# Kernel tuning notes

Measured on AMD Instinct MI355X. Metric: run time of the kernel, lower is better.

The kernel has to match this reference:

```python
import jax, jax.numpy as jnp
from jax import lax
import numpy as np

EPS = 1e-5
K = 3


def _conv(x, w, b, pad, dil=1, groups=1):
    out = lax.conv_general_dilated(
        x, w, (1, 1), [(pad, pad), (pad, pad)], rhs_dilation=(dil, dil),
        dimension_numbers=('NCHW', 'OIHW', 'NCHW'), feature_group_count=groups)
    return out + b[None, :, None, None]


def _bn(x, g, b, m, v):
    scale = g / jnp.sqrt(v + EPS)
    return (x - m[None, :, None, None]) * scale[None, :, None, None] + b[None, :, None, None]


def setup_inputs() -> dict:
    key = jax.random.key(0)
    ks = jax.random.split(key, 24)
    B, C, H, W = 8, 256, 48, 80
    Hd = 256  # hidden_channels
    n = lambda k, s, sc=0.05: (jax.random.normal(k, s, dtype=jnp.float32) * sc)
    return {
        'f_t_minus_2': jax.random.normal(ks[0], (B, C, H, W), dtype=jnp.float32),
        'f_t_minus_1': jax.random.normal(ks[1], (B, C, H, W), dtype=jnp.float32),
        'f_t':         jax.random.normal(ks[2], (B, C, H, W), dtype=jnp.float32),
        'ov_w1': n(ks[3], (Hd, 3 * C, 3, 3)), 'ov_b1': n(ks[4], (Hd,)),
        'bn1_g': jnp.ones((Hd,), jnp.float32), 'bn1_b': jnp.zeros((Hd,), jnp.float32),
        'bn1_m': n(ks[5], (Hd,)), 'bn1_v': jax.random.uniform(ks[6], (Hd,), jnp.float32, 0.5, 1.5),
        'ov_w2': n(ks[7], (Hd, Hd, 3, 3)), 'ov_b2': n(ks[8], (Hd,)),
        'bn2_g': jnp.ones((Hd,), jnp.float32), 'bn2_b': jnp.zeros((Hd,), jnp.float32),
        'bn2_m': n(ks[9], (Hd,)), 'bn2_v': jax.random.uniform(ks[10], (Hd,), jnp.float32, 0.5, 1.5),
        'g_w': n(ks[11], (C, Hd, 1, 1)), 'g_b': n(ks[12], (C,)),
        'fc1_w': n(ks[13], (512, 2 * C)), 'fc1_b': n(ks[14], (512,)),
        'fc2_w': n(ks[15], (C * K * K, 512)), 'fc2_b': n(ks[16], (C * K * K,)),
        'ap_w': n(ks[17], (1, 2 * C, 1, 1)), 'ap_b': n(ks[18], (1,)),
        'a_w': n(ks[19], (1, 2 * C, 1, 1)), 'a_b': jnp.ones((1,), jnp.float32),
    }


def reference(f_t_minus_2, f_t_minus_1, f_t,
              ov_w1, ov_b1, bn1_g, bn1_b, bn1_m, bn1_v,
              ov_w2, ov_b2, bn2_g, bn2_b, bn2_m, bn2_v,
              g_w, g_b, fc1_w, fc1_b, fc2_w, fc2_b,
              ap_w, ap_b, a_w, a_b):
    B, C, H, W = f_t.shape
    # (1) Overview-Net (GCM)
    f_concat = jnp.concatenate([f_t_minus_2, f_t_minus_1, f_t], axis=1)
    h = jax.nn.relu(_bn(_conv(f_concat, ov_w1, ov_b1, pad=2, dil=2), bn1_g, bn1_b, bn1_m, bn1_v))
    h = jax.nn.relu(_bn(_conv(h, ov_w2, ov_b2, pad=4, dil=4), bn2_g, bn2_b, bn2_m, bn2_v))
    g_pooled = h.mean(axis=(2, 3), keepdims=True)            # [B,Hd,1,1]
    G = _conv(g_pooled, g_w, g_b, pad=0)                     # [B,C,1,1]
    # (2) Focus-Net: FC-generated per-(batch,channel) 3x3 depthwise conv on (f_t, f_{t-1})
    Fs = jnp.concatenate([f_t, f_t_minus_1], axis=0)         # [2B,C,H,W]
    g_flat = jnp.repeat(G.reshape(B, C), 2, axis=0)          # [2B,C]
    gap = Fs.mean(axis=(2, 3))                               # [2B,C]
    fc_in = jnp.concatenate([g_flat, gap], axis=1)           # [2B,2C]
    w = jax.nn.silu(fc_in @ fc1_w.T + fc1_b) @ fc2_w.T + fc2_b  # [2B, C*9]
    w = w.reshape(2 * B * C, 1, K, K)
    x = Fs.reshape(1, 2 * B * C, H, W)
    out = lax.conv_general_dilated(
        x, w, (1, 1), [(1, 1), (1, 1)],
        dimension_numbers=('NCHW', 'OIHW', 'NCHW'), feature_group_count=2 * B * C)
    out = out.reshape(2 * B, C, H, W)
    f_t_mod, f_t1_mod = out[:B], out[B:]
    # (3) Dynamic fusion
    f_prev_cat = jnp.concatenate([f_t1_mod, f_t_minus_2], axis=1)
    alpha_prev = 0.3 + 0.4 * jax.nn.sigmoid(_conv(f_prev_cat, ap_w, ap_b, pad=0))
    f_prev = alpha_prev * f_t1_mod + (1.0 - alpha_prev) * f_t_minus_2
    f_cat = jnp.concatenate([f_t_mod, f_prev], axis=1)
    alpha = 0.6 + 0.3 * jax.nn.sigmoid(_conv(f_cat, a_w, a_b, pad=0))
    return alpha * f_t_mod + (1.0 - alpha) * f_prev
```

## Files before the change

kernel.cpp:

```cpp
#include <hip/hip_runtime.h>
#include <hip/hip_bf16.h>
#include <math.h>


typedef __bf16 bf16x8 __attribute__((ext_vector_type(8)));
typedef float f32x4 __attribute__((ext_vector_type(4)));
typedef __attribute__((address_space(1))) void as1_void;
typedef __attribute__((address_space(3))) void as3_void;


__global__ __launch_bounds__(256) void prep_consts_kernel(
    const float* __restrict__ ob1, const float* __restrict__ g1, const float* __restrict__ b1,
    const float* __restrict__ m1, const float* __restrict__ v1,
    const float* __restrict__ ob2, const float* __restrict__ g2, const float* __restrict__ b2,
    const float* __restrict__ m2, const float* __restrict__ v2,
    float* __restrict__ cst)
{
  int i = threadIdx.x;
  float a1 = g1[i] / sqrtf(v1[i] + 1e-5f);
  cst[i]       = a1;
  cst[256 + i] = (ob1[i] - m1[i]) * a1 + b1[i];
  float a2 = g2[i] / sqrtf(v2[i] + 1e-5f);
  cst[512 + i] = a2;
  cst[768 + i] = (ob2[i] - m2[i]) * a2 + b2[i];
}

__global__ __launch_bounds__(256) void pad_concat_kernel(
    const float* __restrict__ f2, const float* __restrict__ f1, const float* __restrict__ f0,
    __hip_bfloat16* __restrict__ out)
{
  int bid = blockIdx.x;
  const int cg = bid % 6; bid /= 6;
  const int y = bid % 48;
  const int b = bid / 48;

  __shared__ float tile[128 * 85];

  const float* src = (cg < 2) ? f2 : ((cg < 4) ? f1 : f0);
  const int ccbase = (cg & 1) * 128;

#pragma unroll
  for (int it = 0; it < 10; it++) {
    const int idx = it * 256 + threadIdx.x;
    const int cl = idx / 20, x4 = idx % 20;
    const float4 v = *(const float4*)(src +
        (((size_t)b * 256 + ccbase + cl) * 48 + y) * 80 + x4 * 4);
    float* t = tile + cl * 85 + x4 * 4;
    t[0] = v.x; t[1] = v.y; t[2] = v.z; t[3] = v.w;
  }
  __syncthreads();

  __hip_bfloat16* obase = out + ((size_t)(b * 52 + y + 2) * 84 + 2) * 768 + cg * 128;
#pragma unroll
  for (int it = 0; it < 5; it++) {
    const int idx = it * 256 + threadIdx.x;
    const int chunk = idx & 15, x = idx >> 4;
    const float* t = tile + chunk * 8 * 85 + x;
    union { __hip_bfloat16 h[8]; uint4 u; } pk;
#pragma unroll
    for (int j = 0; j < 8; j++) pk.h[j] = __float2bfloat16(t[j * 85]);
    *(uint4*)(obase + (size_t)x * 768 + chunk * 8) = pk.u;
  }
}

__global__ __launch_bounds__(256) void repack_w_kernel(
    const float* __restrict__ w, __hip_bfloat16* __restrict__ out, int OC, int IC)
{
  int idx = blockIdx.x * 256 + threadIdx.x;
  if (idx >= OC * IC * 9) return;
  int ic = idx % IC;
  int t = idx / IC;
  int oc = t % OC;
  int tap = t / OC;
  out[idx] = __float2bfloat16(w[(oc * IC + ic) * 9 + tap]);
}

__global__ __launch_bounds__(256) void gap_kernel(
    const float* __restrict__ f0, const float* __restrict__ f1, float* __restrict__ gapv)
{
  int i = blockIdx.x >> 8, c = blockIdx.x & 255;
  const float* src = (i < 8) ? (f0 + ((size_t)i * 256 + c) * 3840)
                             : (f1 + ((size_t)(i - 8) * 256 + c) * 3840);
  float s = 0.f;
  for (int k = threadIdx.x; k < 3840; k += 256) s += src[k];
  for (int off = 32; off; off >>= 1) s += __shfl_xor(s, off);
  __shared__ float red[4];
  if ((threadIdx.x & 63) == 0) red[threadIdx.x >> 6] = s;
  __syncthreads();
  if (threadIdx.x == 0)
    gapv[blockIdx.x] = (red[0] + red[1] + red[2] + red[3]) * (1.f / 3840.f);
}

template <int CIN, int HP, int WP, int DIL, int MODE>
__global__ __launch_bounds__(256) void conv_mfma_kernel(
    const __hip_bfloat16* __restrict__ inp, const __hip_bfloat16* __restrict__ wt,
    const float* __restrict__ bnA, const float* __restrict__ bnB,
    __hip_bfloat16* __restrict__ outp, float* __restrict__ gpool)
{
  __shared__ unsigned short As[8192] __attribute__((aligned(16)));
  __shared__ unsigned short Bs[8192] __attribute__((aligned(16)));

  int bid = blockIdx.x;
  bid = (bid & 7) * 60 + (bid >> 3);
  const int ocb = bid & 1; bid >>= 1;
  const int xb = bid % 5; bid /= 5;
  const int yb = bid % 6; bid /= 6;
  const int b = bid;
  const int y0 = yb * 8, x0 = xb * 16, oc0 = ocb * 128;

  const int t = threadIdx.x;
  const int w = t >> 6, l = t & 63;
  const int col16 = l & 15, quad = l >> 4;
  const int wm = w >> 1, wn = w & 1;
  const int rsub = l >> 3;
  const int jj = (l & 7) ^ rsub;

  f32x4 acc[4][4];
  const f32x4 zf = {0.f, 0.f, 0.f, 0.f};
#pragma unroll
  for (int i = 0; i < 4; i++)
#pragma unroll
    for (int j = 0; j < 4; j++) acc[i][j] = zf;

  for (int c0 = 0; c0 < CIN; c0 += 64) {
    for (int tap = 0; tap < 9; tap++) {
      const int ty = tap / 3, tx = tap - ty * 3;
      const __hip_bfloat16* inBase =
          inp + ((size_t)(b * HP + y0 + DIL * ty) * WP + (x0 + DIL * tx)) * CIN + jj * 8 + c0;
      const __hip_bfloat16* wBase = wt + (size_t)(tap * 256 + oc0) * CIN + jj * 8 + c0;
      __syncthreads();
#pragma unroll
      for (int i = 0; i < 4; i++) {
        const int q = i * 4 + w;
        const int m = q * 8 + rsub;
        const int ry = m >> 4, rx = m & 15;
        const __hip_bfloat16* gp = inBase + (ry * WP + rx) * CIN;
        __builtin_amdgcn_global_load_lds((as1_void*)gp,
            (as3_void*)((char*)As + q * 1024), 16, 0, 0);
      }
#pragma unroll
      for (int i = 0; i < 4; i++) {
        const int q = i * 4 + w;
        const int n = q * 8 + rsub;
        const __hip_bfloat16* gp = wBase + n * CIN;
        __builtin_amdgcn_global_load_lds((as1_void*)gp,
            (as3_void*)((char*)Bs + q * 1024), 16, 0, 0);
      }
      __syncthreads();
#pragma unroll
      for (int kiter = 0; kiter < 2; kiter++) {
        bf16x8 af[4], bg[4];
#pragma unroll
        for (int fi = 0; fi < 4; fi++) {
          const int m = wm * 64 + fi * 16 + col16;
          const int jc = (kiter * 4 + quad) ^ (m & 7);
          af[fi] = *(const bf16x8*)((const char*)As + m * 128 + jc * 16);
        }
#pragma unroll
        for (int fi = 0; fi < 4; fi++) {
          const int n = wn * 64 + fi * 16 + col16;
          const int jc = (kiter * 4 + quad) ^ (n & 7);
          bg[fi] = *(const bf16x8*)((const char*)Bs + n * 128 + jc * 16);
        }
#pragma unroll
        for (int fm_ = 0; fm_ < 4; fm_++)
#pragma unroll
          for (int fn_ = 0; fn_ < 4; fn_++)
            acc[fm_][fn_] = __builtin_amdgcn_mfma_f32_16x16x32_bf16(
                af[fm_], bg[fn_], acc[fm_][fn_], 0, 0, 0);
      }
    }
  }

  if (MODE == 0) {
#pragma unroll
    for (int fn_ = 0; fn_ < 4; fn_++) {
      const int oc = oc0 + wn * 64 + fn_ * 16 + col16;
      const float sa = bnA[oc], sb = bnB[oc];
#pragma unroll
      for (int fm_ = 0; fm_ < 4; fm_++) {
#pragma unroll
        for (int r = 0; r < 4; r++) {
          const int m = wm * 64 + fm_ * 16 + quad * 4 + r;
          const int y = y0 + (m >> 4), x = x0 + (m & 15);
          const float v = fmaxf(acc[fm_][fn_][r] * sa + sb, 0.f);
          outp[((size_t)(b * 56 + y + 4) * 88 + (x + 4)) * 256 + oc] = __float2bfloat16(v);
        }
      }
    }
  } else {
#pragma unroll
    for (int fn_ = 0; fn_ < 4; fn_++) {
      const int oc = oc0 + wn * 64 + fn_ * 16 + col16;
      const float sa = bnA[oc], sb = bnB[oc];
      float cs = 0.f;
#pragma unroll
      for (int fm_ = 0; fm_ < 4; fm_++)
#pragma unroll
        for (int r = 0; r < 4; r++)
          cs += fmaxf(acc[fm_][fn_][r] * sa + sb, 0.f);
      cs += __shfl_xor(cs, 16);
      cs += __shfl_xor(cs, 32);
      if (quad == 0) atomicAdd(&gpool[b * 256 + oc], cs);
    }
  }
}


__global__ __launch_bounds__(256) void fcG_kernel(
    const float* __restrict__ gpool, const float* __restrict__ gw,
    const float* __restrict__ gb, float* __restrict__ G)
{
  int b = blockIdx.x, oc = threadIdx.x;
  __shared__ float pool[256];
  pool[oc] = gpool[b * 256 + oc] * (1.f / 3840.f);
  __syncthreads();
  float s = gb[oc];
  const float* wr = gw + oc * 256;
  for (int c2 = 0; c2 < 256; c2++) s += pool[c2] * wr[c2];
  G[b * 256 + oc] = s;
}

__global__ __launch_bounds__(256) void fc1_kernel(
    const float* __restrict__ G, const float* __restrict__ gapv,
    const float* __restrict__ w, const float* __restrict__ bias,
    float* __restrict__ out1)
{
  __shared__ float fin[16][513];
  for (int idx = threadIdx.x; idx < 16 * 512; idx += 256) {
    int i = idx >> 9, k = idx & 511;
    fin[i][k] = (k < 256) ? G[(i >> 1) * 256 + k] : gapv[i * 256 + (k - 256)];
  }
  __syncthreads();
  int g = blockIdx.x * 256 + threadIdx.x;
  int j = g >> 4, i = g & 15;
  float s = bias[j];
  const float* wr = w + j * 512;
  for (int k = 0; k < 512; k++) s += fin[i][k] * wr[k];
  out1[j * 16 + i] = s / (1.f + expf(-s));
}

__global__ __launch_bounds__(256) void fc2_kernel(
    const float* __restrict__ out1, const float* __restrict__ w,
    const float* __restrict__ bias, float* __restrict__ wdw)
{
  __shared__ float fin[16][513];
  for (int idx = threadIdx.x; idx < 16 * 512; idx += 256) {
    int i = idx >> 9, k = idx & 511;
    fin[i][k] = out1[k * 16 + i];
  }
  __syncthreads();
  int g = blockIdx.x * 256 + threadIdx.x;
  int j = g >> 4, i = g & 15;
  float s = bias[j];
  const float* wr = w + j * 512;
  for (int k = 0; k < 512; k++) s += fin[i][k] * wr[k];
  wdw[i * 2304 + j] = s;
}

__global__ __launch_bounds__(256) void dw_kernel(
    const float* __restrict__ f0, const float* __restrict__ f1,
    const float* __restrict__ wdw, float* __restrict__ fm)
{
  int i = blockIdx.x >> 8, c = blockIdx.x & 255;
  const float* src = (i < 8) ? (f0 + ((size_t)i * 256 + c) * 3840)
                             : (f1 + ((size_t)(i - 8) * 256 + c) * 3840);
  float* dst = fm + ((size_t)i * 256 + c) * 3840;
  __shared__ float w9[9];
  if (threadIdx.x < 9) w9[threadIdx.x] = wdw[i * 2304 + c * 9 + threadIdx.x];
  __syncthreads();
  for (int p = threadIdx.x; p < 3840; p += 256) {
    int y = p / 80, x = p - y * 80;
    float s = 0.f;
#pragma unroll
    for (int ky = 0; ky < 3; ky++) {
      int yy = y + ky - 1;
      if (yy < 0 || yy >= 48) continue;
#pragma unroll
      for (int kx = 0; kx < 3; kx++) {
        int xx = x + kx - 1;
        if (xx < 0 || xx >= 80) continue;
        s += w9[ky * 3 + kx] * src[yy * 80 + xx];
      }
    }
    dst[p] = s;
  }
}

__global__ __launch_bounds__(320) void alpha_final_kernel(
    const float* __restrict__ fm, const float* __restrict__ f2,
    const float* __restrict__ apw, const float* __restrict__ apb,
    const float* __restrict__ aw, const float* __restrict__ ab,
    float* __restrict__ out)
{
  int b = blockIdx.x / 48, y = blockIdx.x % 48;
  int x = threadIdx.x % 80, g = threadIdx.x / 80;
  const float* ftm  = fm + ((size_t)b * 256) * 3840 + y * 80 + x;
  const float* ft1m = fm + ((size_t)(b + 8) * 256) * 3840 + y * 80 + x;
  const float* ptm2 = f2 + ((size_t)b * 256) * 3840 + y * 80 + x;
  float S = 0.f, T0 = 0.f, T1 = 0.f, T2 = 0.f;
  for (int cc = 0; cc < 64; cc++) {
    int c = g * 64 + cc;
    float v1 = ft1m[(size_t)c * 3840];
    float v2 = ptm2[(size_t)c * 3840];
    float v0 = ftm[(size_t)c * 3840];
    S  += apw[c] * v1 + apw[256 + c] * v2;
    T0 += aw[c] * v0;
    T1 += aw[256 + c] * v1;
    T2 += aw[256 + c] * v2;
  }
  __shared__ float red[4][4][80];
  __shared__ float apl[80], all[80];
  red[0][g][x] = S; red[1][g][x] = T0; red[2][g][x] = T1; red[3][g][x] = T2;
  __syncthreads();
  if (g == 0) {
    S  = red[0][0][x] + red[0][1][x] + red[0][2][x] + red[0][3][x];
    T0 = red[1][0][x] + red[1][1][x] + red[1][2][x] + red[1][3][x];
    T1 = red[2][0][x] + red[2][1][x] + red[2][2][x] + red[2][3][x];
    T2 = red[3][0][x] + red[3][1][x] + red[3][2][x] + red[3][3][x];
    float ap = 0.3f + 0.4f / (1.f + expf(-(S + apb[0])));
    float A  = T0 + ap * T1 + (1.f - ap) * T2 + ab[0];
    float al = 0.6f + 0.3f / (1.f + expf(-A));
    apl[x] = ap; all[x] = al;
  }
  __syncthreads();
  const float ap = apl[x], al = all[x];
  float* ob = out + ((size_t)b * 256) * 3840 + y * 80 + x;
  for (int cc = 0; cc < 64; cc++) {
    size_t off = (size_t)(g * 64 + cc) * 3840;
    float v0 = ftm[off], v1 = ft1m[off], v2 = ptm2[off];
    ob[off] = al * v0 + (1.f - al) * (ap * v1 + (1.f - ap) * v2);
  }
}


extern "C" void kernel_launch(void* const* d_in, const int* in_sizes, int n_in,
                              void* d_out, int out_size, void* d_ws, size_t ws_size,
                              hipStream_t stream)
{
  const float* f_tm2 = (const float*)d_in[0];
  const float* f_tm1 = (const float*)d_in[1];
  const float* f_t   = (const float*)d_in[2];
  const float* ov_w1 = (const float*)d_in[3];
  const float* ov_b1 = (const float*)d_in[4];
  const float* bn1_g = (const float*)d_in[5];
  const float* bn1_b = (const float*)d_in[6];
  const float* bn1_m = (const float*)d_in[7];
  const float* bn1_v = (const float*)d_in[8];
  const float* ov_w2 = (const float*)d_in[9];
  const float* ov_b2 = (const float*)d_in[10];
  const float* bn2_g = (const float*)d_in[11];
  const float* bn2_b = (const float*)d_in[12];
  const float* bn2_m = (const float*)d_in[13];
  const float* bn2_v = (const float*)d_in[14];
  const float* g_w   = (const float*)d_in[15];
  const float* g_b   = (const float*)d_in[16];
  const float* fc1_w = (const float*)d_in[17];
  const float* fc1_b = (const float*)d_in[18];
  const float* fc2_w = (const float*)d_in[19];
  const float* fc2_b = (const float*)d_in[20];
  const float* ap_w  = (const float*)d_in[21];
  const float* ap_b  = (const float*)d_in[22];
  const float* a_w   = (const float*)d_in[23];
  const float* a_b   = (const float*)d_in[24];

  char* ws = (char*)d_ws;
  float* fm            = (float*)ws;
  __hip_bfloat16* in1p = (__hip_bfloat16*)ws;
  __hip_bfloat16* wt1  = (__hip_bfloat16*)(ws + 53673984);
  __hip_bfloat16* wt2  = (__hip_bfloat16*)(ws + 57212928);
  __hip_bfloat16* h1p  = (__hip_bfloat16*)(ws + 58392576);
  float* gpool         = (float*)(ws + 78577664);
  float* gapv          = (float*)(ws + 78585856);
  float* Gv            = (float*)(ws + 78602240);
  float* out1          = (float*)(ws + 78610432);
  float* wdw           = (float*)(ws + 78643200);
  float* cst           = (float*)(ws + 79036416);

  hipMemsetAsync(in1p, 0, 53673984, stream);
  hipMemsetAsync(h1p, 0, 20185088, stream);
  hipMemsetAsync(gpool, 0, 8192, stream);

  prep_consts_kernel<<<1, 256, 0, stream>>>(ov_b1, bn1_g, bn1_b, bn1_m, bn1_v,
                                            ov_b2, bn2_g, bn2_b, bn2_m, bn2_v, cst);
  pad_concat_kernel<<<2304, 256, 0, stream>>>(f_tm2, f_tm1, f_t, in1p);
  repack_w_kernel<<<6912, 256, 0, stream>>>(ov_w1, wt1, 256, 768);
  repack_w_kernel<<<2304, 256, 0, stream>>>(ov_w2, wt2, 256, 256);
  gap_kernel<<<4096, 256, 0, stream>>>(f_t, f_tm1, gapv);

  conv_mfma_kernel<768, 52, 84, 2, 0><<<480, 256, 0, stream>>>(in1p, wt1, cst, cst + 256, h1p, nullptr);
  conv_mfma_kernel<256, 56, 88, 4, 1><<<480, 256, 0, stream>>>(h1p, wt2, cst + 512, cst + 768, nullptr, gpool);

  fcG_kernel<<<8, 256, 0, stream>>>(gpool, g_w, g_b, Gv);
  fc1_kernel<<<32, 256, 0, stream>>>(Gv, gapv, fc1_w, fc1_b, out1);
  fc2_kernel<<<144, 256, 0, stream>>>(out1, fc2_w, fc2_b, wdw);
  dw_kernel<<<4096, 256, 0, stream>>>(f_t, f_tm1, wdw, fm);
  alpha_final_kernel<<<384, 320, 0, stream>>>(fm, f_tm2, ap_w, ap_b, a_w, a_b, (float*)d_out);
}
```

Before: 528.9 us.

## Fuse GAP into pad_concat, zero only borders, cache alpha inputs in registers

Drops the full 53MB memset of the padded input buffer. pad_concat now zeroes only the border columns and rows it owns, and also computes the spatial sums of f_t and f_{t-1} per channel with atomics. This removes the separate gap_kernel pass over those tensors. The final alpha kernel now uses 640 threads and keeps its 32-channel slice in registers, so the three inputs are not read twice from global memory. The risks are higher register pressure, and the gpool memset now covers gapv, which depends on the workspace layout staying contiguous.

```diff
diff --git a/kernel.cpp b/kernel.cpp
--- a/kernel.cpp
+++ b/kernel.cpp
@@ -27,7 +27,7 @@
 
 __global__ __launch_bounds__(256) void pad_concat_kernel(
     const float* __restrict__ f2, const float* __restrict__ f1, const float* __restrict__ f0,
-    __hip_bfloat16* __restrict__ out)
+    __hip_bfloat16* __restrict__ out, float* __restrict__ gapv)
 {
   int bid = blockIdx.x;
   const int cg = bid % 6; bid /= 6;
@@ -38,6 +38,7 @@
 
   const float* src = (cg < 2) ? f2 : ((cg < 4) ? f1 : f0);
   const int ccbase = (cg & 1) * 128;
+  const uint4 z4 = {0u, 0u, 0u, 0u};
 
 #pragma unroll
   for (int it = 0; it < 10; it++) {
@@ -48,6 +49,20 @@
     float* t = tile + cl * 85 + x4 * 4;
     t[0] = v.x; t[1] = v.y; t[2] = v.z; t[3] = v.w;
   }
+
+  if (threadIdx.x < 32) {
+    const int xb_ = threadIdx.x >> 3, ch8 = threadIdx.x & 7;
+    const int xx = (xb_ < 2) ? xb_ : (80 + xb_);
+    *(uint4*)(out + ((size_t)(b * 52 + y + 2) * 84 + xx) * 768 + cg * 128 + ch8 * 8) = z4;
+  }
+  if (y == 0 || y == 47) {
+    const int r0 = (y == 0) ? 0 : 50;
+    for (int idx = threadIdx.x; idx < 1344; idx += 256) {
+      const int rr = idx / 672, rem = idx % 672;
+      const int xx = rem >> 3, ch8 = rem & 7;
+      *(uint4*)(out + ((size_t)(b * 52 + r0 + rr) * 84 + xx) * 768 + cg * 128 + ch8 * 8) = z4;
+    }
+  }
   __syncthreads();
 
   __hip_bfloat16* obase = out + ((size_t)(b * 52 + y + 2) * 84 + 2) * 768 + cg * 128;
@@ -60,6 +75,17 @@
 #pragma unroll
     for (int j = 0; j < 8; j++) pk.h[j] = __float2bfloat16(t[j * 85]);
     *(uint4*)(obase + (size_t)x * 768 + chunk * 8) = pk.u;
+  }
+
+  if (cg >= 2) {
+    const int i_gap = (cg >= 4) ? b : (b + 8);
+    const int cl = threadIdx.x >> 1, half = threadIdx.x & 1;
+    const float* t = tile + cl * 85 + half * 40;
+    float s = 0.f;
+#pragma unroll
+    for (int k = 0; k < 40; k++) s += t[k];
+    s += __shfl_xor(s, 1);
+    if (half == 0) atomicAdd(&gapv[i_gap * 256 + ccbase + cl], s);
   }
 }
 
@@ -73,22 +99,6 @@
   int oc = t % OC;
   int tap = t / OC;
   out[idx] = __float2bfloat16(w[(oc * IC + ic) * 9 + tap]);
-}
-
-__global__ __launch_bounds__(256) void gap_kernel(
-    const float* __restrict__ f0, const float* __restrict__ f1, float* __restrict__ gapv)
-{
-  int i = blockIdx.x >> 8, c = blockIdx.x & 255;
-  const float* src = (i < 8) ? (f0 + ((size_t)i * 256 + c) * 3840)
-                             : (f1 + ((size_t)(i - 8) * 256 + c) * 3840);
-  float s = 0.f;
-  for (int k = threadIdx.x; k < 3840; k += 256) s += src[k];
-  for (int off = 32; off; off >>= 1) s += __shfl_xor(s, off);
-  __shared__ float red[4];
-  if ((threadIdx.x & 63) == 0) red[threadIdx.x >> 6] = s;
-  __syncthreads();
-  if (threadIdx.x == 0)
-    gapv[blockIdx.x] = (red[0] + red[1] + red[2] + red[3]) * (1.f / 3840.f);
 }
 
 template <int CIN, int HP, int WP, int DIL, int MODE>
@@ -229,7 +239,8 @@
   __shared__ float fin[16][513];
   for (int idx = threadIdx.x; idx < 16 * 512; idx += 256) {
     int i = idx >> 9, k = idx & 511;
-    fin[i][k] = (k < 256) ? G[(i >> 1) * 256 + k] : gapv[i * 256 + (k - 256)];
+    fin[i][k] = (k < 256) ? G[(i >> 1) * 256 + k]
+                          : gapv[i * 256 + (k - 256)] * (1.f / 3840.f);
   }
   __syncthreads();
   int g = blockIdx.x * 256 + threadIdx.x;
@@ -287,7 +298,7 @@
   }
 }
 
-__global__ __launch_bounds__(320) void alpha_final_kernel(
+__global__ __launch_bounds__(640) void alpha_final_kernel(
     const float* __restrict__ fm, const float* __restrict__ f2,
     const float* __restrict__ apw, const float* __restrict__ apb,
     const float* __restrict__ aw, const float* __restrict__ ab,
@@ -295,42 +306,44 @@
 {
   int b = blockIdx.x / 48, y = blockIdx.x % 48;
   int x = threadIdx.x % 80, g = threadIdx.x / 80;
-  const float* ftm  = fm + ((size_t)b * 256) * 3840 + y * 80 + x;
-  const float* ft1m = fm + ((size_t)(b + 8) * 256) * 3840 + y * 80 + x;
-  const float* ptm2 = f2 + ((size_t)b * 256) * 3840 + y * 80 + x;
+  const float* ftm  = fm + ((size_t)(b * 256) + g * 32) * 3840 + y * 80 + x;
+  const float* ft1m = fm + ((size_t)((b + 8) * 256) + g * 32) * 3840 + y * 80 + x;
+  const float* ptm2 = f2 + ((size_t)(b * 256) + g * 32) * 3840 + y * 80 + x;
+
+  float v0[32], v1[32], v2[32];
   float S = 0.f, T0 = 0.f, T1 = 0.f, T2 = 0.f;
-  for (int cc = 0; cc < 64; cc++) {
-    int c = g * 64 + cc;
-    float v1 = ft1m[(size_t)c * 3840];
-    float v2 = ptm2[(size_t)c * 3840];
-    float v0 = ftm[(size_t)c * 3840];
-    S  += apw[c] * v1 + apw[256 + c] * v2;
-    T0 += aw[c] * v0;
-    T1 += aw[256 + c] * v1;
-    T2 += aw[256 + c] * v2;
-  }
-  __shared__ float red[4][4][80];
-  __shared__ float apl[80], all[80];
+#pragma unroll
+  for (int cc = 0; cc < 32; cc++) {
+    v0[cc] = ftm[(size_t)cc * 3840];
+    v1[cc] = ft1m[(size_t)cc * 3840];
+    v2[cc] = ptm2[(size_t)cc * 3840];
+    const int c = g * 32 + cc;
+    S  += apw[c] * v1[cc] + apw[256 + c] * v2[cc];
+    T0 += aw[c] * v0[cc];
+    T1 += aw[256 + c] * v1[cc];
+    T2 += aw[256 + c] * v2[cc];
+  }
+  __shared__ float red[4][8][80];
+  __shared__ float apl[80], alb[80];
   red[0][g][x] = S; red[1][g][x] = T0; red[2][g][x] = T1; red[3][g][x] = T2;
   __syncthreads();
   if (g == 0) {
-    S  = red[0][0][x] + red[0][1][x] + red[0][2][x] + red[0][3][x];
-    T0 = red[1][0][x] + red[1][1][x] + red[1][2][x] + red[1][3][x];
-    T1 = red[2][0][x] + red[2][1][x] + red[2][2][x] + red[2][3][x];
-    T2 = red[3][0][x] + red[3][1][x] + red[3][2][x] + red[3][3][x];
-    float ap = 0.3f + 0.4f / (1.f + expf(-(S + apb[0])));
-    float A  = T0 + ap * T1 + (1.f - ap) * T2 + ab[0];
+    float s = 0.f, t0 = 0.f, t1 = 0.f, t2 = 0.f;
+#pragma unroll
+    for (int k = 0; k < 8; k++) {
+      s += red[0][k][x]; t0 += red[1][k][x]; t1 += red[2][k][x]; t2 += red[3][k][x];
+    }
+    float ap = 0.3f + 0.4f / (1.f + expf(-(s + apb[0])));
+    float A  = t0 + ap * t1 + (1.f - ap) * t2 + ab[0];
     float al = 0.6f + 0.3f / (1.f + expf(-A));
-    apl[x] = ap; all[x] = al;
-  }
-  __syncthreads();
-  const float ap = apl[x], al = all[x];
-  float* ob = out + ((size_t)b * 256) * 3840 + y * 80 + x;
-  for (int cc = 0; cc < 64; cc++) {
-    size_t off = (size_t)(g * 64 + cc) * 3840;
-    float v0 = ftm[off], v1 = ft1m[off], v2 = ptm2[off];
-    ob[off] = al * v0 + (1.f - al) * (ap * v1 + (1.f - ap) * v2);
-  }
+    apl[x] = ap; alb[x] = al;
+  }
+  __syncthreads();
+  const float ap = apl[x], al = alb[x];
+  float* ob = out + ((size_t)(b * 256) + g * 32) * 3840 + y * 80 + x;
+#pragma unroll
+  for (int cc = 0; cc < 32; cc++)
+    ob[(size_t)cc * 3840] = al * v0[cc] + (1.f - al) * (ap * v1[cc] + (1.f - ap) * v2[cc]);
 }
 
 
@@ -377,16 +390,14 @@
   float* wdw           = (float*)(ws + 78643200);
   float* cst           = (float*)(ws + 79036416);
 
-  hipMemsetAsync(in1p, 0, 53673984, stream);
   hipMemsetAsync(h1p, 0, 20185088, stream);
-  hipMemsetAsync(gpool, 0, 8192, stream);
+  hipMemsetAsync(gpool, 0, 24576, stream);
 
   prep_consts_kernel<<<1, 256, 0, stream>>>(ov_b1, bn1_g, bn1_b, bn1_m, bn1_v,
                                             ov_b2, bn2_g, bn2_b, bn2_m, bn2_v, cst);
-  pad_concat_kernel<<<2304, 256, 0, stream>>>(f_tm2, f_tm1, f_t, in1p);
+  pad_concat_kernel<<<2304, 256, 0, stream>>>(f_tm2, f_tm1, f_t, in1p, gapv);
   repack_w_kernel<<<6912, 256, 0, stream>>>(ov_w1, wt1, 256, 768);
   repack_w_kernel<<<2304, 256, 0, stream>>>(ov_w2, wt2, 256, 256);
-  gap_kernel<<<4096, 256, 0, stream>>>(f_t, f_tm1, gapv);
 
   conv_mfma_kernel<768, 52, 84, 2, 0><<<480, 256, 0, stream>>>(in1p, wt1, cst, cst + 256, h1p, nullptr);
   conv_mfma_kernel<256, 56, 88, 4, 1><<<480, 256, 0, stream>>>(h1p, wt2, cst + 512, cst + 768, nullptr, gpool);
@@ -395,5 +406,5 @@
   fc1_kernel<<<32, 256, 0, stream>>>(Gv, gapv, fc1_w, fc1_b, out1);
   fc2_kernel<<<144, 256, 0, stream>>>(out1, fc2_w, fc2_b, wdw);
   dw_kernel<<<4096, 256, 0, stream>>>(f_t, f_tm1, wdw, fm);
-  alpha_final_kernel<<<384, 320, 0, stream>>>(fm, f_tm2, ap_w, ap_b, a_w, a_b, (float*)d_out);
-}
+  alpha_final_kernel<<<384, 640, 0, stream>>>(fm, f_tm2, ap_w, ap_b, a_w, a_b, (float*)d_out);
+}
```

Result: faster. 508.3 us (-3.9%).
